# Performance work log

Measured on AMD Instinct MI355X. Metric: run time of the kernel, lower is better.

## Reference

```python
import jax, jax.numpy as jnp
import numpy as np
from jax import lax

BS, L, H = 8, 2048, 1024
NH, HD = 16, 64


def setup_inputs() -> dict:
    key = jax.random.key(0)
    ks = jax.random.split(key, 4)
    s = 1.0 / np.sqrt(H)
    xav = np.sqrt(2.0 / (NH + HD))  # xavier_normal_ for ReadingHead (fan_in=HD? torch uses dims (NH,HD))
    return {
        "hidden_states": jax.random.normal(ks[0], (BS, L, H), jnp.float32),
        "K1_w": jax.random.normal(ks[1], (H, NH * HD), jnp.float32) * s,
        "K1_b": jnp.zeros((NH * HD,), jnp.float32),
        "V1_w": jax.random.normal(ks[2], (H, NH * HD), jnp.float32) * s,
        "V1_b": jnp.zeros((NH * HD,), jnp.float32),
        "bidirection_weight": jnp.full((1, 1, NH, 1, 4), 0.25, jnp.float32),
        "ReadingHead": jax.random.normal(ks[3], (NH, HD), jnp.float32) * xav,
    }


def _nearest_valid_maps(valid, L):
    # valid: [bs, L, nh] bool. Returns fm, bm: [bs, L, 2, nh] int32, matching the
    # original sequential torch loop (including its use of len_index = L-1-j for the
    # backward map's slot 0).
    bs, _, nh = valid.shape
    mask_t = jnp.moveaxis(valid, 1, 0)  # [L, bs, nh]

    def step(carry, x):
        a, b = carry
        m, v = x
        nb = jnp.where(m, a, b)
        na = jnp.where(m, v, a)
        return (na, nb), (na, nb)

    zero = jnp.zeros((bs, nh), jnp.int32)
    idx_fwd = jnp.arange(1, L, dtype=jnp.int32)
    _, (fa, fb) = lax.scan(step, (zero, zero), (mask_t[1:], idx_fwd))
    fa = jnp.concatenate([zero[None], fa], axis=0)  # [L, bs, nh]
    fb = jnp.concatenate([zero[None], fb], axis=0)

    last = jnp.full((bs, nh), L - 1, jnp.int32)
    # backward loop stores len_index = L-1-j at position j when valid
    vals_bwd = (L - 1) - jnp.arange(L - 1, dtype=jnp.int32)
    _, (ba, bb) = lax.scan(step, (last, last), (mask_t[: L - 1], vals_bwd), reverse=True)
    ba = jnp.concatenate([ba, last[None]], axis=0)
    bb = jnp.concatenate([bb, last[None]], axis=0)

    fm = jnp.stack([fa, fb], axis=2).transpose(1, 0, 2, 3)  # [bs, L, 2, nh]
    bm = jnp.stack([ba, bb], axis=2).transpose(1, 0, 2, 3)
    return fm, bm


def reference(hidden_states, K1_w, K1_b, V1_w, V1_b, bidirection_weight, ReadingHead):
    bs, length, _ = hidden_states.shape
    nh, hd = ReadingHead.shape
    K1 = jax.nn.relu(hidden_states @ K1_w + K1_b).reshape(bs, length, nh, hd)
    V1 = jax.nn.relu(hidden_states @ V1_w + V1_b).reshape(bs, length, nh, hd)
    dots = jnp.einsum('blnh,nh->bln', K1, ReadingHead)
    valid = dots > 0.5
    fm, bm = _nearest_valid_maps(valid, length)
    # gather V along sequence dim with the two nearest-valid maps
    Vf = jnp.take_along_axis(V1, fm.reshape(bs, 2 * length, nh, 1), axis=1)
    Vf = Vf.reshape(bs, length, 2, nh, hd)
    Vb = jnp.take_along_axis(V1, bm.reshape(bs, 2 * length, nh, 1), axis=1)
    Vb = Vb.reshape(bs, length, 2, nh, hd)
    # [bs, L, 4, nh, hd] -> [bs, L, nh, hd, 4], weighted sum over the 4 registers
    new_states = jnp.concatenate([Vf, Vb], axis=2).transpose(0, 1, 3, 4, 2) * bidirection_weight
    context = new_states.sum(axis=-1).reshape(bs, length, nh * hd)
    return context
```

## Files before the change

kernel.cpp:

```cpp
#include <hip/hip_runtime.h>
#include <hip/hip_bf16.h>
#include <cstdint>

#define BS 8
#define SEQ 2048
#define HDIM 1024
#define NH 16
#define HD 64
#define M_ROWS (BS * SEQ)
#define N_COLS (2 * HDIM)
#define KDIM HDIM

#define DELTA 0.025f
#define FLAG_CAP 32768

#define OFF_A      ((size_t)0)
#define OFF_BT     ((size_t)33554432)
#define OFF_FCNT   ((size_t)37748736)
#define OFF_FLIST  ((size_t)37748800)
#define OFF_BIAS   ((size_t)37879872)
#define OFF_CVH    ((size_t)41943040)
#define OFF_VALID  ((size_t)75497472)
#define OFF_MAPS   ((size_t)75759616)

typedef __attribute__((ext_vector_type(8))) __bf16 bf16x8;
typedef __attribute__((ext_vector_type(4))) float f32x4;

__device__ __forceinline__ unsigned short f2bf(float f) {
    unsigned int x = __builtin_bit_cast(unsigned int, f);
    unsigned int r = x + 0x7fffu + ((x >> 16) & 1u);
    return (unsigned short)(r >> 16);
}
__device__ __forceinline__ float bf2f(unsigned short u) {
    return __builtin_bit_cast(float, (unsigned int)u << 16);
}

__device__ __forceinline__ void g2l16(const void* gp, void* lp) {
    __builtin_amdgcn_global_load_lds(
        (__attribute__((address_space(1))) void*)(void*)gp,
        (__attribute__((address_space(3))) void*)lp, 16, 0, 0);
}

__global__ __launch_bounds__(256) void prep_kernel(const float4* __restrict__ hs4,
                                                   unsigned short* __restrict__ Abf,
                                                   const float* __restrict__ K1w,
                                                   const float* __restrict__ V1w,
                                                   unsigned short* __restrict__ Bt,
                                                   const float* __restrict__ K1b,
                                                   const float* __restrict__ V1b,
                                                   float* __restrict__ bias,
                                                   int* __restrict__ fcnt) {
    __shared__ float tile[32][33];
    const int blk = blockIdx.x;
    const int t = threadIdx.x;
    if (blk < 8192) {
        int i = blk * 256 + t;
        float4 v0 = hs4[i * 2];
        float4 v1 = hs4[i * 2 + 1];
        uint4 o;
        o.x = (unsigned)f2bf(v0.x) | ((unsigned)f2bf(v0.y) << 16);
        o.y = (unsigned)f2bf(v0.z) | ((unsigned)f2bf(v0.w) << 16);
        o.z = (unsigned)f2bf(v1.x) | ((unsigned)f2bf(v1.y) << 16);
        o.w = (unsigned)f2bf(v1.z) | ((unsigned)f2bf(v1.w) << 16);
        ((uint4*)Abf)[i] = o;
    } else if (blk < 10240) {
        int lb = blk - 8192;
        int z = lb >> 10;
        int tk = (lb >> 5) & 31;
        int tn = lb & 31;
        const float* W = z ? V1w : K1w;
        int r = t >> 3;
        int c4 = (t & 7) * 4;
        const float4 v = *(const float4*)&W[(size_t)(tk * 32 + r) * 1024 + tn * 32 + c4];
        tile[r][c4 + 0] = v.x; tile[r][c4 + 1] = v.y;
        tile[r][c4 + 2] = v.z; tile[r][c4 + 3] = v.w;
        __syncthreads();
        int n = tn * 32 + r;
        int k = tk * 32 + c4;
        ushort4 o;
        o.x = f2bf(tile[c4 + 0][r]); o.y = f2bf(tile[c4 + 1][r]);
        o.z = f2bf(tile[c4 + 2][r]); o.w = f2bf(tile[c4 + 3][r]);
        *(ushort4*)&Bt[((size_t)z * 1024 + n) * 1024 + k] = o;
    } else {
        int i = (blk - 10240) * 256 + t;
        bias[i] = (i < 1024) ? K1b[i] : V1b[i - 1024];
        if (i == 0) *fcnt = 0;
    }
}

__global__ __launch_bounds__(256) void gemm_kernel(const unsigned short* __restrict__ Abf,
                                                   const unsigned short* __restrict__ Btbf,
                                                   const float* __restrict__ bias,
                                                   const float* __restrict__ RH,
                                                   unsigned short* __restrict__ CVh,
                                                   unsigned char* __restrict__ valid,
                                                   int* __restrict__ fcnt,
                                                   int* __restrict__ flist) {
    constexpr int K = KDIM, BK = 64;
    __shared__ unsigned short As[128 * BK];
    __shared__ unsigned short Bs[128 * BK];
    const int t = threadIdx.x;
    const int wave = t >> 6, lane = t & 63;
    const int wm = wave >> 1, wn = wave & 1;
    const int l16 = lane & 15, quad = lane >> 4;
    const int sw = l16 & 7;

    const int wgid = blockIdx.y * 16 + blockIdx.x;
    const int swz = (wgid & 7) * 256 + (wgid >> 3);
    const int m0 = (swz >> 4) * 128, n0 = (swz & 15) * 128;

    f32x4 zero4 = {0.f, 0.f, 0.f, 0.f};
    f32x4 acc[4][4];
#pragma unroll
    for (int i = 0; i < 4; i++)
#pragma unroll
        for (int j = 0; j < 4; j++) acc[i][j] = zero4;

    const int rr = t >> 3;
    const int gsw = (t ^ (t >> 3)) & 7;
    const unsigned short* gA = Abf + (size_t)(m0 + rr) * K + gsw * 8;
    const unsigned short* gB = Btbf + (size_t)(n0 + rr) * K + gsw * 8;
    char* lAs = (char*)As + (size_t)wave * 1024;
    char* lBs = (char*)Bs + (size_t)wave * 1024;

    for (int k0 = 0; k0 < K; k0 += BK) {
#pragma unroll
        for (int i = 0; i < 4; i++)
            g2l16(gA + (size_t)i * 32 * K + k0, lAs + i * 4096);
#pragma unroll
        for (int i = 0; i < 4; i++)
            g2l16(gB + (size_t)i * 32 * K + k0, lBs + i * 4096);
        __syncthreads();
#pragma unroll
        for (int h = 0; h < 2; h++) {
            bf16x8 af[4], bfr[4];
            const int hq = h * 4 + quad;
#pragma unroll
            for (int mt = 0; mt < 4; mt++)
                af[mt] = *(const bf16x8*)&As[(wm * 64 + mt * 16 + l16) * BK + (hq ^ sw) * 8];
#pragma unroll
            for (int nt = 0; nt < 4; nt++)
                bfr[nt] = *(const bf16x8*)&Bs[(wn * 64 + nt * 16 + l16) * BK + (hq ^ sw) * 8];
#pragma unroll
            for (int mt = 0; mt < 4; mt++)
#pragma unroll
                for (int nt = 0; nt < 4; nt++)
                    acc[mt][nt] = __builtin_amdgcn_mfma_f32_16x16x32_bf16(af[mt], bfr[nt], acc[mt][nt], 0, 0, 0);
        }
        __syncthreads();
    }
    if (n0 < HDIM) {
        const int n = (n0 >> 6) + wn;
        float rh[4], bv[4];
#pragma unroll
        for (int nt = 0; nt < 4; nt++) {
            int col = n * 64 + nt * 16 + l16;
            rh[nt] = RH[col];
            bv[nt] = bias[col];
        }
#pragma unroll
        for (int mt = 0; mt < 4; mt++) {
#pragma unroll
            for (int r = 0; r < 4; r++) {
                float p = 0.f;
#pragma unroll
                for (int nt = 0; nt < 4; nt++)
                    p += fmaxf(acc[mt][nt][r] + bv[nt], 0.f) * rh[nt];
#pragma unroll
                for (int s = 8; s >= 1; s >>= 1) p += __shfl_xor(p, s, 64);
                if (l16 == 0) {
                    int row = m0 + wm * 64 + mt * 16 + quad * 4 + r;
                    int b = row >> 11, l = row & (SEQ - 1);
                    valid[((size_t)b * NH + n) * SEQ + l] = (p > 0.5f) ? 1 : 0;
                    if (fabsf(p - 0.5f) < DELTA) {
                        int idx = atomicAdd(fcnt, 1);
                        if (idx < FLAG_CAP) flist[idx] = row * NH + n;
                    }
                }
            }
        }
    } else {
        const int nv0 = n0 - HDIM;
#pragma unroll
        for (int mt = 0; mt < 4; mt++) {
            int gm = m0 + wm * 64 + mt * 16 + quad * 4;
#pragma unroll
            for (int nt = 0; nt < 4; nt++) {
                int gn = nv0 + wn * 64 + nt * 16 + l16;
                float bvv = bias[HDIM + gn];
#pragma unroll
                for (int r = 0; r < 4; r++)
                    CVh[(size_t)(gm + r) * HDIM + gn] = f2bf(fmaxf(acc[mt][nt][r] + bvv, 0.f));
            }
        }
    }
}

__global__ __launch_bounds__(256) void refine_kernel(const float* __restrict__ hs,
                                                     const float* __restrict__ K1w,
                                                     const float* __restrict__ K1b,
                                                     const float* __restrict__ RH,
                                                     const int* __restrict__ fcnt,
                                                     const int* __restrict__ flist,
                                                     unsigned char* __restrict__ valid) {
    int cnt = *fcnt;
    if (cnt > FLAG_CAP) cnt = FLAG_CAP;
    const int wave = threadIdx.x >> 6, d = threadIdx.x & 63;
    const int task = blockIdx.x * 4 + wave;
    if (task >= cnt) return;

    const int code = flist[task];
    const int n = code & (NH - 1);
    const int bl = code >> 4;
    const float* x = hs + (size_t)bl * HDIM;
    const float* wp = K1w + n * 64 + d;

    double acc0 = 0.0, acc1 = 0.0, acc2 = 0.0, acc3 = 0.0;
    for (int k = 0; k < KDIM; k += 32) {
        float w[32];
#pragma unroll
        for (int u = 0; u < 32; u++)
            w[u] = wp[(size_t)(k + u) * 1024];
        float4 xv[8];
#pragma unroll
        for (int u = 0; u < 8; u++)
            xv[u] = *(const float4*)(x + k + u * 4);
#pragma unroll
        for (int u = 0; u < 8; u++) {
            acc0 += (double)xv[u].x * (double)w[u * 4 + 0];
            acc1 += (double)xv[u].y * (double)w[u * 4 + 1];
            acc2 += (double)xv[u].z * (double)w[u * 4 + 2];
            acc3 += (double)xv[u].w * (double)w[u * 4 + 3];
        }
    }
    double k1 = ((acc0 + acc1) + (acc2 + acc3)) + (double)K1b[n * 64 + d];
    if (k1 < 0.0) k1 = 0.0;
    double contrib = k1 * (double)RH[n * 64 + d];
#pragma unroll
    for (int s = 32; s >= 1; s >>= 1) contrib += __shfl_xor(contrib, s, 64);
    if (d == 0) {
        int b = bl >> 11, l = bl & (SEQ - 1);
        valid[((size_t)b * NH + n) * SEQ + l] = (contrib > 0.5) ? 1 : 0;
    }
}

__global__ __launch_bounds__(64) void scan_kernel(const unsigned char* __restrict__ valid,
                                                  ushort4* __restrict__ maps) {
    int bn = blockIdx.x;
    int b = bn >> 4, n = bn & (NH - 1);
    int lane = threadIdx.x;
    __shared__ unsigned int summ[64];

    const unsigned char* vp = valid + (size_t)bn * SEQ + lane * 32;
    uint4 c0 = *(const uint4*)vp;
    uint4 c1 = *(const uint4*)(vp + 16);
    unsigned int wds[8] = {c0.x, c0.y, c0.z, c0.w, c1.x, c1.y, c1.z, c1.w};
    unsigned int mask = 0;
#pragma unroll
    for (int i = 0; i < 8; i++) {
#pragma unroll
        for (int j = 0; j < 4; j++)
            mask |= (((wds[i] >> (8 * j)) & 0xffu) ? 1u : 0u) << (i * 4 + j);
    }

    int cnt = 0, va = 0, vb = 0;
#pragma unroll
    for (int tt = 0; tt < 32; tt++) {
        if (mask & (1u << tt)) { vb = va; va = lane * 32 + tt; cnt++; }
    }
    summ[lane] = (unsigned)((cnt > 2 ? 2 : cnt) | (va << 2) | (vb << 13));
    __syncthreads();
    int a = 0, bb_ = 0;
    for (int tt = 0; tt < lane; tt++) {
        unsigned s = summ[tt];
        int c = s & 3, sva = (s >> 2) & 2047, svb = (s >> 13) & 2047;
        if (c >= 2) { a = sva; bb_ = svb; }
        else if (c == 1) { bb_ = a; a = sva; }
    }
    unsigned int fres[32];
#pragma unroll
    for (int tt = 0; tt < 32; tt++) {
        if (mask & (1u << tt)) { bb_ = a; a = lane * 32 + tt; }
        fres[tt] = (unsigned)a | ((unsigned)bb_ << 16);
    }
    __syncthreads();

    unsigned int maskb = mask;
    if (lane == 63) maskb &= ~(1u << 31);
    cnt = 0; va = 0; vb = 0;
#pragma unroll
    for (int tt = 31; tt >= 0; tt--) {
        if (maskb & (1u << tt)) { vb = va; va = (SEQ - 1) - (lane * 32 + tt); cnt++; }
    }
    summ[lane] = (unsigned)((cnt > 2 ? 2 : cnt) | (va << 2) | (vb << 13));
    __syncthreads();
    int a2 = SEQ - 1, b2 = SEQ - 1;
    for (int tt = 63; tt > lane; tt--) {
        unsigned s = summ[tt];
        int c = s & 3, sva = (s >> 2) & 2047, svb = (s >> 13) & 2047;
        if (c >= 2) { a2 = sva; b2 = svb; }
        else if (c == 1) { b2 = a2; a2 = sva; }
    }
#pragma unroll
    for (int tt = 31; tt >= 0; tt--) {
        int j = lane * 32 + tt;
        if (maskb & (1u << tt)) { b2 = a2; a2 = (SEQ - 1) - j; }
        unsigned f = fres[tt];
        maps[((size_t)b * SEQ + j) * NH + n] =
            make_ushort4((unsigned short)(f & 0xffffu), (unsigned short)(f >> 16),
                         (unsigned short)a2, (unsigned short)b2);
    }
}

__global__ __launch_bounds__(256) void gather_kernel(const unsigned short* __restrict__ CVh,
                                                     const ushort4* __restrict__ maps,
                                                     const float* __restrict__ bw,
                                                     float* __restrict__ out) {
    int bl = blockIdx.x;
    int t = threadIdx.x, n = t >> 4, q = t & 15;
    int b = bl >> 11;
    ushort4 m = maps[(size_t)bl * NH + n];
    const float4 w = *(const float4*)&bw[n * 4];
    size_t colbase = (size_t)(n * 64 + q * 4);
    size_t rowb = (size_t)b * SEQ;
    const ushort4 u0 = *(const ushort4*)&CVh[(rowb + m.x) * HDIM + colbase];
    const ushort4 u1 = *(const ushort4*)&CVh[(rowb + m.y) * HDIM + colbase];
    const ushort4 u2 = *(const ushort4*)&CVh[(rowb + m.z) * HDIM + colbase];
    const ushort4 u3 = *(const ushort4*)&CVh[(rowb + m.w) * HDIM + colbase];
    float4 o;
    o.x = w.x * bf2f(u0.x) + w.y * bf2f(u1.x) + w.z * bf2f(u2.x) + w.w * bf2f(u3.x);
    o.y = w.x * bf2f(u0.y) + w.y * bf2f(u1.y) + w.z * bf2f(u2.y) + w.w * bf2f(u3.y);
    o.z = w.x * bf2f(u0.z) + w.y * bf2f(u1.z) + w.z * bf2f(u2.z) + w.w * bf2f(u3.z);
    o.w = w.x * bf2f(u0.w) + w.y * bf2f(u1.w) + w.z * bf2f(u2.w) + w.w * bf2f(u3.w);
    *(float4*)&out[(size_t)bl * (NH * HD) + n * 64 + q * 4] = o;
}

extern "C" void kernel_launch(void* const* d_in, const int* in_sizes, int n_in,
                              void* d_out, int out_size, void* d_ws, size_t ws_size,
                              hipStream_t stream) {
    (void)in_sizes; (void)n_in; (void)out_size; (void)ws_size;
    const float* hs  = (const float*)d_in[0];
    const float* K1w = (const float*)d_in[1];
    const float* K1b = (const float*)d_in[2];
    const float* V1w = (const float*)d_in[3];
    const float* V1b = (const float*)d_in[4];
    const float* bw  = (const float*)d_in[5];
    const float* RH  = (const float*)d_in[6];
    float* out = (float*)d_out;
    char* ws = (char*)d_ws;

    unsigned short* Abf  = (unsigned short*)(ws + OFF_A);
    unsigned short* Btbf = (unsigned short*)(ws + OFF_BT);
    int* fcnt = (int*)(ws + OFF_FCNT);
    int* flist = (int*)(ws + OFF_FLIST);
    float* bias  = (float*)(ws + OFF_BIAS);
    unsigned short* CVh = (unsigned short*)(ws + OFF_CVH);
    unsigned char* valid = (unsigned char*)(ws + OFF_VALID);
    ushort4* maps = (ushort4*)(ws + OFF_MAPS);

    prep_kernel<<<10248, 256, 0, stream>>>((const float4*)hs, Abf,
                                           K1w, V1w, Btbf, K1b, V1b, bias, fcnt);
    gemm_kernel<<<dim3(N_COLS / 128, M_ROWS / 128), 256, 0, stream>>>(
        Abf, Btbf, bias, RH, CVh, valid, fcnt, flist);
    refine_kernel<<<FLAG_CAP / 4, 256, 0, stream>>>(
        hs, K1w, K1b, RH, fcnt, flist, valid);
    scan_kernel<<<BS * NH, 64, 0, stream>>>(valid, maps);
    gather_kernel<<<BS * SEQ, 256, 0, stream>>>(CVh, maps, bw, out);
}
```

Before: 372.9 us.

## Bucket flagged rows per head and share staged K1 weight slice in refine

The single global flag list becomes 16 per-head lists, each with its own counter and a cap of 2048 entries. The refine kernel now runs a fixed grid of 32 blocks per head with 512 threads each. Each block stages its head's K1 weight slice through LDS in 128-row chunks so that 8 waves, one flagged row each, reuse it. Before, every wave re-read the weight column from global memory, and most of the 8192 launched blocks exited early. The trade-offs are extra block-wide barriers, and a correctness risk: rows past 2048 in any one head are silently dropped instead of hitting the old shared 32768 cap.

```diff
diff --git a/kernel.cpp b/kernel.cpp
--- a/kernel.cpp
+++ b/kernel.cpp
@@ -12,7 +12,7 @@
 #define KDIM HDIM
 
 #define DELTA 0.025f
-#define FLAG_CAP 32768
+#define PERH_CAP 2048
 
 #define OFF_A      ((size_t)0)
 #define OFF_BT     ((size_t)33554432)
@@ -84,7 +84,7 @@
     } else {
         int i = (blk - 10240) * 256 + t;
         bias[i] = (i < 1024) ? K1b[i] : V1b[i - 1024];
-        if (i == 0) *fcnt = 0;
+        if (i < 16) fcnt[i] = 0;
     }
 }
 
@@ -173,8 +173,8 @@
                     int b = row >> 11, l = row & (SEQ - 1);
                     valid[((size_t)b * NH + n) * SEQ + l] = (p > 0.5f) ? 1 : 0;
                     if (fabsf(p - 0.5f) < DELTA) {
-                        int idx = atomicAdd(fcnt, 1);
-                        if (idx < FLAG_CAP) flist[idx] = row * NH + n;
+                        int idx = atomicAdd(&fcnt[n], 1);
+                        if (idx < PERH_CAP) flist[n * PERH_CAP + idx] = row;
                     }
                 }
             }
@@ -196,51 +196,71 @@
     }
 }
 
-__global__ __launch_bounds__(256) void refine_kernel(const float* __restrict__ hs,
+__global__ __launch_bounds__(512) void refine_kernel(const float* __restrict__ hs,
                                                      const float* __restrict__ K1w,
                                                      const float* __restrict__ K1b,
                                                      const float* __restrict__ RH,
                                                      const int* __restrict__ fcnt,
                                                      const int* __restrict__ flist,
                                                      unsigned char* __restrict__ valid) {
-    int cnt = *fcnt;
-    if (cnt > FLAG_CAP) cnt = FLAG_CAP;
+    __shared__ float Wl[128 * 64];
+    const int n = blockIdx.x >> 5;
+    const int g = blockIdx.x & 31;
     const int wave = threadIdx.x >> 6, d = threadIdx.x & 63;
-    const int task = blockIdx.x * 4 + wave;
-    if (task >= cnt) return;
-
-    const int code = flist[task];
-    const int n = code & (NH - 1);
-    const int bl = code >> 4;
-    const float* x = hs + (size_t)bl * HDIM;
-    const float* wp = K1w + n * 64 + d;
-
-    double acc0 = 0.0, acc1 = 0.0, acc2 = 0.0, acc3 = 0.0;
-    for (int k = 0; k < KDIM; k += 32) {
-        float w[32];
-#pragma unroll
-        for (int u = 0; u < 32; u++)
-            w[u] = wp[(size_t)(k + u) * 1024];
-        float4 xv[8];
-#pragma unroll
-        for (int u = 0; u < 8; u++)
-            xv[u] = *(const float4*)(x + k + u * 4);
-#pragma unroll
-        for (int u = 0; u < 8; u++) {
-            acc0 += (double)xv[u].x * (double)w[u * 4 + 0];
-            acc1 += (double)xv[u].y * (double)w[u * 4 + 1];
-            acc2 += (double)xv[u].z * (double)w[u * 4 + 2];
-            acc3 += (double)xv[u].w * (double)w[u * 4 + 3];
-        }
-    }
-    double k1 = ((acc0 + acc1) + (acc2 + acc3)) + (double)K1b[n * 64 + d];
-    if (k1 < 0.0) k1 = 0.0;
-    double contrib = k1 * (double)RH[n * 64 + d];
-#pragma unroll
-    for (int s = 32; s >= 1; s >>= 1) contrib += __shfl_xor(contrib, s, 64);
-    if (d == 0) {
-        int b = bl >> 11, l = bl & (SEQ - 1);
-        valid[((size_t)b * NH + n) * SEQ + l] = (contrib > 0.5) ? 1 : 0;
+    int cnt = fcnt[n];
+    if (cnt > PERH_CAP) cnt = PERH_CAP;
+
+    const int r0 = threadIdx.x >> 4;
+    const int c4 = (threadIdx.x & 15) * 4;
+    const float bn = K1b[n * 64 + d];
+    const float rhn = RH[n * 64 + d];
+
+    for (int base = g * 8; base < cnt; base += 32 * 8) {
+        const int task = base + wave;
+        const bool live = task < cnt;
+        const int bl = live ? flist[n * PERH_CAP + task] : 0;
+        const float* x = hs + (size_t)bl * HDIM;
+
+        double acc0 = 0.0, acc1 = 0.0, acc2 = 0.0, acc3 = 0.0;
+        for (int kc = 0; kc < KDIM; kc += 128) {
+#pragma unroll
+            for (int rr = 0; rr < 4; rr++) {
+                const float4 v = *(const float4*)&K1w[(size_t)(kc + rr * 32 + r0) * 1024 + n * 64 + c4];
+                *(float4*)&Wl[(rr * 32 + r0) * 64 + c4] = v;
+            }
+            __syncthreads();
+            if (live) {
+                for (int k = 0; k < 128; k += 32) {
+                    float w[32];
+#pragma unroll
+                    for (int u = 0; u < 32; u++)
+                        w[u] = Wl[(k + u) * 64 + d];
+                    float4 xv[8];
+#pragma unroll
+                    for (int u = 0; u < 8; u++)
+                        xv[u] = *(const float4*)(x + kc + k + u * 4);
+#pragma unroll
+                    for (int u = 0; u < 8; u++) {
+                        acc0 += (double)xv[u].x * (double)w[u * 4 + 0];
+                        acc1 += (double)xv[u].y * (double)w[u * 4 + 1];
+                        acc2 += (double)xv[u].z * (double)w[u * 4 + 2];
+                        acc3 += (double)xv[u].w * (double)w[u * 4 + 3];
+                    }
+                }
+            }
+            __syncthreads();
+        }
+        if (live) {
+            double k1 = ((acc0 + acc1) + (acc2 + acc3)) + (double)bn;
+            if (k1 < 0.0) k1 = 0.0;
+            double contrib = k1 * (double)rhn;
+#pragma unroll
+            for (int s = 32; s >= 1; s >>= 1) contrib += __shfl_xor(contrib, s, 64);
+            if (d == 0) {
+                int b = bl >> 11, l = bl & (SEQ - 1);
+                valid[((size_t)b * NH + n) * SEQ + l] = (contrib > 0.5) ? 1 : 0;
+            }
+        }
     }
 }
 
@@ -362,7 +382,7 @@
                                            K1w, V1w, Btbf, K1b, V1b, bias, fcnt);
     gemm_kernel<<<dim3(N_COLS / 128, M_ROWS / 128), 256, 0, stream>>>(
         Abf, Btbf, bias, RH, CVh, valid, fcnt, flist);
-    refine_kernel<<<FLAG_CAP / 4, 256, 0, stream>>>(
+    refine_kernel<<<NH * 32, 512, 0, stream>>>(
         hs, K1w, K1b, RH, fcnt, flist, valid);
     scan_kernel<<<BS * NH, 64, 0, stream>>>(valid, maps);
     gather_kernel<<<BS * SEQ, 256, 0, stream>>>(CVh, maps, bw, out);
```

Result: faster. 350.3 us (-6.1%).
